# Performance work log

Measured on AMD Instinct MI355X. Metric: run time of the kernel, lower is better.

## Reference

```python
import jax, jax.numpy as jnp
import numpy as np

B, L, D, NLAYERS, KCONV = 8, 2048, 1024, 3, 4


def setup_inputs() -> dict:
    key = jax.random.key(0)
    ks = jax.random.split(key, 8)
    inp = {
        "x": jax.random.normal(ks[0], (B, L, D), jnp.float32),
        "conv_w": jax.random.normal(ks[1], (NLAYERS, D, KCONV), jnp.float32) * 0.02,
        "conv_b": jnp.zeros((NLAYERS, D), jnp.float32),
        "wr_w": jax.random.normal(ks[2], (NLAYERS, D, D), jnp.float32) * (1.0 / np.sqrt(D)),
        "wr_b": jnp.zeros((NLAYERS, D), jnp.float32),
        "wi_w": jax.random.normal(ks[3], (NLAYERS, D, D), jnp.float32) * (1.0 / np.sqrt(D)),
        "wi_b": jnp.zeros((NLAYERS, D), jnp.float32),
        "log_a": 3.0 + 0.1 * jax.random.normal(ks[4], (NLAYERS, D), jnp.float32),
        "wo_w": jax.random.normal(ks[5], (NLAYERS, D, D), jnp.float32) * (1.0 / np.sqrt(D)),
        "norm_w": jnp.ones((NLAYERS, D), jnp.float32),
        "norm_out_w": jnp.ones((D,), jnp.float32),
    }
    return inp


def _rmsnorm(x, w, eps=1e-6):
    return x * w * jax.lax.rsqrt(jnp.mean(x * x, axis=-1, keepdims=True) + eps)


def _parallel_scan(a, b):
    # h_t = a_t * h_{t-1} + b_t  via log-space prefix scan (h0 = 0)
    a32 = a.astype(jnp.float32)
    b32 = b.astype(jnp.float32)
    log_A = jnp.cumsum(jnp.log(jnp.maximum(a32, 1e-7)), axis=1)
    log_A = jnp.maximum(log_A, -80.0)  # a<=1 so log_A<=0 already
    A = jnp.exp(log_A)
    h = A * jnp.cumsum(b32 * jnp.exp(-log_A), axis=1)
    return h.astype(a.dtype)


def _rglru_layer(x, cw, cb, wrw, wrb, wiw, wib, la, wow, nw):
    # causal depthwise conv1d, kernel 4, left pad 3
    Lx = x.shape[1]
    xp = jnp.pad(x, ((0, 0), (KCONV - 1, 0), (0, 0)))
    x_conv = cb + sum(xp[:, k:k + Lx, :] * cw[:, k] for k in range(KCONV))
    r_t = jax.nn.sigmoid(x_conv @ wrw.T + wrb)
    i_t = jax.nn.sigmoid(x_conv @ wiw.T + wib)
    a_base = jax.nn.sigmoid(la.astype(jnp.float32)).astype(x.dtype)
    a_t = a_base ** (8.0 * r_t)
    b_t = jnp.sqrt(jnp.clip(1.0 - a_t * a_t, 1e-6, None)) * (i_t * x_conv)
    h = _parallel_scan(a_t, b_t)
    return _rmsnorm(h @ wow.T, nw)


def reference(x, conv_w, conv_b, wr_w, wr_b, wi_w, wi_b, log_a, wo_w, norm_w, norm_out_w):
    h = x
    for l in range(NLAYERS):
        h = _rglru_layer(h, conv_w[l], conv_b[l], wr_w[l], wr_b[l],
                         wi_w[l], wi_b[l], log_a[l], wo_w[l], norm_w[l])
    return _rmsnorm(h, norm_out_w)
```

## Files before the change

### kernel.cpp

```cpp
#include <hip/hip_runtime.h>
#include <type_traits>

#define BDIM 8
#define LDIM 2048
#define DDIM 1024
#define NL 3
#define K4 4
#define MDIM (BDIM * LDIM)
#define BK 64
#define NT (DDIM / BK)

typedef __bf16 bf16x8 __attribute__((ext_vector_type(8)));
typedef __bf16 bf16x4 __attribute__((ext_vector_type(4)));
typedef float f32x4 __attribute__((ext_vector_type(4)));
typedef const __attribute__((address_space(1))) void gvoid_t;
typedef __attribute__((address_space(3))) void svoid_t;

__device__ __forceinline__ void load16(const void* g, void* lds_uniform) {
    __builtin_amdgcn_global_load_lds((gvoid_t*)g, (svoid_t*)lds_uniform, 16, 0, 0);
}

#define SBAR()                                  \
    do {                                        \
        asm volatile("" ::: "memory");          \
        __builtin_amdgcn_s_barrier();           \
        asm volatile("" ::: "memory");          \
    } while (0)
#define WAITV(N) asm volatile("s_waitcnt vmcnt(" #N ")" ::: "memory")

__global__ void cvt_bf16(const float* __restrict__ s, __bf16* __restrict__ d, int n) {
    int i = blockIdx.x * 256 + threadIdx.x;
    if (i < n) d[i] = (__bf16)s[i];
}

__global__ __launch_bounds__(256) void cvt_interleave(const float* __restrict__ wr,
                                                      const float* __restrict__ wi,
                                                      __bf16* __restrict__ w2, int n) {
    int i = blockIdx.x * 256 + threadIdx.x;
    if (i >= n) return;
    int k = i & (DDIM - 1);
    int ld = i >> 10;
    int l = ld >> 10;
    int d = ld & (DDIM - 1);
    size_t base = ((size_t)l * 2 * DDIM + 2 * d) * DDIM + k;
    w2[base] = (__bf16)wr[i];
    w2[base + DDIM] = (__bf16)wi[i];
}

template <typename T>
__global__ __launch_bounds__(256) void conv_kernel(const T* __restrict__ X,
                                                   const float* __restrict__ cw,
                                                   const float* __restrict__ cb,
                                                   __bf16* __restrict__ XC) {
    int idx = blockIdx.x * 256 + threadIdx.x;
    int d = (idx & (DDIM / 4 - 1)) << 2;
    int t = (idx >> 8) & (LDIM - 1);
    int b = idx >> 19;
    float wv[4][4];
    *(float4*)wv[0] = ((const float4*)cw)[d + 0];
    *(float4*)wv[1] = ((const float4*)cw)[d + 1];
    *(float4*)wv[2] = ((const float4*)cw)[d + 2];
    *(float4*)wv[3] = ((const float4*)cw)[d + 3];
    float4 cbv = *(const float4*)(cb + d);
    float acc[4] = {cbv.x, cbv.y, cbv.z, cbv.w};
#pragma unroll
    for (int k = 0; k < K4; k++) {
        int tt = t + k - (K4 - 1);
        if (tt >= 0) {
            size_t off = ((size_t)(b * LDIM + tt) << 10) + d;
            float xv[4];
            if constexpr (std::is_same<T, float>::value) {
                float4 v = *(const float4*)(X + off);
                xv[0] = v.x; xv[1] = v.y; xv[2] = v.z; xv[3] = v.w;
            } else {
                bf16x4 v = *(const bf16x4*)(X + off);
                xv[0] = (float)v.x; xv[1] = (float)v.y; xv[2] = (float)v.z; xv[3] = (float)v.w;
            }
#pragma unroll
            for (int j = 0; j < 4; j++) acc[j] += xv[j] * wv[j][k];
        }
    }
    bf16x4 o;
    o.x = (__bf16)acc[0]; o.y = (__bf16)acc[1]; o.z = (__bf16)acc[2]; o.w = (__bf16)acc[3];
    *(bf16x4*)(XC + ((size_t)(b * LDIM + t) << 10) + d) = o;
}

__global__ __launch_bounds__(512, 2) void gate_gemm(
    const __bf16* __restrict__ A, const __bf16* __restrict__ W2,
    const float* __restrict__ wrb, const float* __restrict__ wib,
    const float* __restrict__ la,
    __bf16* __restrict__ LOGA, __bf16* __restrict__ BB) {
    __shared__ __attribute__((aligned(16))) __bf16 sm[4][16384];
    int tid = threadIdx.x;
    int wave = tid >> 6, lane = tid & 63;
    int wm = wave >> 2, wn = wave & 3;
    int fr = lane & 15, quad = lane >> 4;

    int nx = gridDim.x;
    int bid = blockIdx.y * nx + blockIdx.x;
    int cpx = (nx * gridDim.y) >> 3;
    int sw = (bid & 7) * cpx + (bid >> 3);
    int bm0 = (sw / nx) * 256;
    int bn0 = (sw % nx) * 256;

    const __bf16* Ag = A + (size_t)bm0 * DDIM;
    const __bf16* Bg = W2 + (size_t)bn0 * DDIM;

    f32x4 acc[8][4];
    f32x4 zero = {0.f, 0.f, 0.f, 0.f};
#pragma unroll
    for (int i = 0; i < 8; i++)
#pragma unroll
        for (int j = 0; j < 4; j++) acc[i][j] = zero;

    auto STAGE = [&](int buf, int ko) {
#pragma unroll
        for (int h = 0; h < 2; h++)
#pragma unroll
            for (int j = 0; j < 2; j++) {
                int ci = j * 512 + tid;
                int r = ci >> 3;
                int g = (ci & 7) ^ (r & 7);
                size_t go = (size_t)(h * 128 + r) * DDIM + ko + g * 8;
                int lb = h * 8192 + j * 4096 + wave * 512;
                load16(Ag + go, &sm[buf * 2][lb]);
                load16(Bg + go, &sm[buf * 2 + 1][lb]);
            }
    };

    STAGE(0, 0);
    int c = 0;
    for (int t = 0; t < NT; t++) {
        SBAR();
        if (t + 1 < NT) {
            STAGE(c ^ 1, (t + 1) * BK);
            WAITV(8);
        } else {
            WAITV(0);
        }
        SBAR();
        const __bf16* Ac = sm[c * 2];
        const __bf16* Bc = sm[c * 2 + 1];
#pragma unroll
        for (int ph = 0; ph < 4; ph++) {
            if (ph) SBAR();
            const int mh = ph & 1, kw = ph >> 1;
            bf16x8 af[4], bfm[4];
#pragma unroll
            for (int mi = 0; mi < 4; mi++) {
                int row = wm * 128 + (mh * 4 + mi) * 16 + fr;
                af[mi] = *(const bf16x8*)(Ac + row * 64 + ((kw * 4 + quad) ^ (row & 7)) * 8);
            }
#pragma unroll
            for (int ni = 0; ni < 4; ni++) {
                int row = wn * 64 + ni * 16 + fr;
                bfm[ni] = *(const bf16x8*)(Bc + row * 64 + ((kw * 4 + quad) ^ (row & 7)) * 8);
            }
            __builtin_amdgcn_s_setprio(1);
#pragma unroll
            for (int ni = 0; ni < 4; ni++)
#pragma unroll
                for (int mi = 0; mi < 4; mi++)
                    acc[mh * 4 + mi][ni] = __builtin_amdgcn_mfma_f32_16x16x32_bf16(
                        af[mi], bfm[ni], acc[mh * 4 + mi][ni], 0, 0, 0);
            __builtin_amdgcn_s_setprio(0);
        }
        c ^= 1;
    }

    float* Lt = (float*)&sm[0][0];
    int colg = (tid & 31) * 8;
    int d0 = (bn0 >> 1) + (colg >> 1);
    float rb[4], ibv[4], lnab[4];
    {
        float4 r4 = *(const float4*)(wrb + d0);
        float4 i4 = *(const float4*)(wib + d0);
        float4 l4 = *(const float4*)(la + d0);
        float lav[4] = {l4.x, l4.y, l4.z, l4.w};
        rb[0] = r4.x; rb[1] = r4.y; rb[2] = r4.z; rb[3] = r4.w;
        ibv[0] = i4.x; ibv[1] = i4.y; ibv[2] = i4.z; ibv[3] = i4.w;
#pragma unroll
        for (int j = 0; j < 4; j++) lnab[j] = __logf(1.f / (1.f + __expf(-lav[j])));
    }
#pragma unroll
    for (int mi = 0; mi < 8; mi++) {
        __syncthreads();
#pragma unroll
        for (int ni = 0; ni < 4; ni++) {
            int col = wn * 64 + ni * 16 + fr;
#pragma unroll
            for (int reg = 0; reg < 4; reg++)
                Lt[(wm * 16 + quad * 4 + reg) * 260 + col] = acc[mi][ni][reg];
        }
        __syncthreads();
#pragma unroll
        for (int hf = 0; hf < 2; hf++) {
            int r = (tid >> 5) + hf * 16;
            int m = bm0 + (r >> 4) * 128 + mi * 16 + (r & 15);
            float vv[8];
            *(f32x4*)&vv[0] = *(const f32x4*)&Lt[r * 260 + colg];
            *(f32x4*)&vv[4] = *(const f32x4*)&Lt[r * 260 + colg + 4];
            bf16x4 xcv = *(const bf16x4*)(A + (size_t)m * DDIM + d0);
            bf16x4 og, ob;
#pragma unroll
            for (int j = 0; j < 4; j++) {
                float rv = 1.f / (1.f + __expf(-(vv[2 * j] + rb[j])));
                float iv = 1.f / (1.f + __expf(-(vv[2 * j + 1] + ibv[j])));
                float lga = 8.f * rv * lnab[j];
                float a = __expf(lga);
                float bt = sqrtf(fmaxf(1.f - a * a, 1e-6f)) * (iv * (float)xcv[j]);
                og[j] = (__bf16)lga;
                ob[j] = (__bf16)bt;
            }
            *(bf16x4*)(LOGA + (size_t)m * DDIM + d0) = og;
            *(bf16x4*)(BB + (size_t)m * DDIM + d0) = ob;
        }
    }
}

__global__ __launch_bounds__(512, 2) void out_gemm(
    const __bf16* __restrict__ A, const __bf16* __restrict__ Wo, __bf16* __restrict__ HW) {
    __shared__ __attribute__((aligned(16))) __bf16 sm[4][16384];
    int tid = threadIdx.x;
    int wave = tid >> 6, lane = tid & 63;
    int wm = wave >> 2, wn = wave & 3;
    int fr = lane & 15, quad = lane >> 4;

    int nx = gridDim.x;
    int bid = blockIdx.y * nx + blockIdx.x;
    int cpx = (nx * gridDim.y) >> 3;
    int sw = (bid & 7) * cpx + (bid >> 3);
    int bm0 = (sw / nx) * 256;
    int bn0 = (sw % nx) * 256;

    const __bf16* Ag = A + (size_t)bm0 * DDIM;
    const __bf16* Bg = Wo + (size_t)bn0 * DDIM;

    f32x4 acc[8][4];
    f32x4 zero = {0.f, 0.f, 0.f, 0.f};
#pragma unroll
    for (int i = 0; i < 8; i++)
#pragma unroll
        for (int j = 0; j < 4; j++) acc[i][j] = zero;

    auto STAGE = [&](int buf, int ko) {
#pragma unroll
        for (int h = 0; h < 2; h++)
#pragma unroll
            for (int j = 0; j < 2; j++) {
                int ci = j * 512 + tid;
                int r = ci >> 3;
                int g = (ci & 7) ^ (r & 7);
                size_t go = (size_t)(h * 128 + r) * DDIM + ko + g * 8;
                int lb = h * 8192 + j * 4096 + wave * 512;
                load16(Ag + go, &sm[buf * 2][lb]);
                load16(Bg + go, &sm[buf * 2 + 1][lb]);
            }
    };

    STAGE(0, 0);
    int c = 0;
    for (int t = 0; t < NT; t++) {
        SBAR();
        if (t + 1 < NT) {
            STAGE(c ^ 1, (t + 1) * BK);
            WAITV(8);
        } else {
            WAITV(0);
        }
        SBAR();
        const __bf16* Ac = sm[c * 2];
        const __bf16* Bc = sm[c * 2 + 1];
#pragma unroll
        for (int ph = 0; ph < 4; ph++) {
            if (ph) SBAR();
            const int mh = ph & 1, kw = ph >> 1;
            bf16x8 af[4], bfm[4];
#pragma unroll
            for (int mi = 0; mi < 4; mi++) {
                int row = wm * 128 + (mh * 4 + mi) * 16 + fr;
                af[mi] = *(const bf16x8*)(Ac + row * 64 + ((kw * 4 + quad) ^ (row & 7)) * 8);
            }
#pragma unroll
            for (int ni = 0; ni < 4; ni++) {
                int row = wn * 64 + ni * 16 + fr;
                bfm[ni] = *(const bf16x8*)(Bc + row * 64 + ((kw * 4 + quad) ^ (row & 7)) * 8);
            }
            __builtin_amdgcn_s_setprio(1);
#pragma unroll
            for (int ni = 0; ni < 4; ni++)
#pragma unroll
                for (int mi = 0; mi < 4; mi++)
                    acc[mh * 4 + mi][ni] = __builtin_amdgcn_mfma_f32_16x16x32_bf16(
                        af[mi], bfm[ni], acc[mh * 4 + mi][ni], 0, 0, 0);
            __builtin_amdgcn_s_setprio(0);
        }
        c ^= 1;
    }

    float* Lt = (float*)&sm[0][0];
    int colg = (tid & 31) * 8;
    int n0 = bn0 + colg;
#pragma unroll
    for (int mi = 0; mi < 8; mi++) {
        __syncthreads();
#pragma unroll
        for (int ni = 0; ni < 4; ni++) {
            int col = wn * 64 + ni * 16 + fr;
#pragma unroll
            for (int reg = 0; reg < 4; reg++)
                Lt[(wm * 16 + quad * 4 + reg) * 260 + col] = acc[mi][ni][reg];
        }
        __syncthreads();
#pragma unroll
        for (int hf = 0; hf < 2; hf++) {
            int r = (tid >> 5) + hf * 16;
            int m = bm0 + (r >> 4) * 128 + mi * 16 + (r & 15);
            float vv[8];
            *(f32x4*)&vv[0] = *(const f32x4*)&Lt[r * 260 + colg];
            *(f32x4*)&vv[4] = *(const f32x4*)&Lt[r * 260 + colg + 4];
            bf16x8 o;
#pragma unroll
            for (int j = 0; j < 8; j++) o[j] = (__bf16)vv[j];
            *(bf16x8*)(HW + (size_t)m * DDIM + n0) = o;
        }
    }
}

#define SC_T (LDIM / 8)
__global__ __launch_bounds__(256) void scan_kernel(const __bf16* __restrict__ LOGA,
                                                   const __bf16* __restrict__ BB,
                                                   __bf16* __restrict__ H) {
    int b = blockIdx.y;
    int dl = threadIdx.x & 31;
    int d = blockIdx.x * 32 + dl;
    int c = threadIdx.x >> 5;
    size_t base = ((size_t)b * LDIM + (size_t)c * SC_T) * DDIM + d;
    const __bf16* pga = LOGA + base;
    const __bf16* pbb = BB + base;
    __bf16* pH = H + base;

    float S = 0.f;
#pragma unroll 8
    for (int t = 0; t < SC_T; t++) S += (float)pga[(size_t)t * DDIM];
    __shared__ float sS[8][32];
    sS[c][dl] = S;
    __syncthreads();
    float L0 = 0.f;
    for (int cc = 0; cc < c; cc++) L0 += sS[cc][dl];

    float Lr = L0, lcp = fmaxf(L0, -80.f), hB = 0.f;
#pragma unroll 4
    for (int t = 0; t < SC_T; t++) {
        float lga = (float)pga[(size_t)t * DDIM];
        Lr += lga;
        float lc = fmaxf(Lr, -80.f);
        hB = __expf(lc - lcp) * hB + (float)pbb[(size_t)t * DDIM];
        lcp = lc;
    }
    float Ac = __expf(fmaxf(Lr, -80.f) - fmaxf(L0, -80.f));
    __shared__ float sA[8][32], sB[8][32];
    sA[c][dl] = Ac;
    sB[c][dl] = hB;
    __syncthreads();
    float hin = 0.f;
    for (int cc = 0; cc < c; cc++) hin = sA[cc][dl] * hin + sB[cc][dl];

    Lr = L0;
    lcp = fmaxf(L0, -80.f);
    float h = hin;
#pragma unroll 4
    for (int t = 0; t < SC_T; t++) {
        float lga = (float)pga[(size_t)t * DDIM];
        Lr += lga;
        float lc = fmaxf(Lr, -80.f);
        h = __expf(lc - lcp) * h + (float)pbb[(size_t)t * DDIM];
        lcp = lc;
        pH[(size_t)t * DDIM] = (__bf16)h;
    }
}

template <typename TI, typename TO>
__global__ __launch_bounds__(256) void rmsnorm_kernel(const TI* __restrict__ X,
                                                      const float* __restrict__ w,
                                                      TO* __restrict__ Y) {
    int row = blockIdx.x;
    int tid = threadIdx.x;
    size_t off = (size_t)row * DDIM + tid * 4;
    float v[4];
    if constexpr (std::is_same<TI, float>::value) {
        float4 t = *(const float4*)(X + off);
        v[0] = t.x; v[1] = t.y; v[2] = t.z; v[3] = t.w;
    } else {
        bf16x4 t = *(const bf16x4*)(X + off);
        v[0] = (float)t.x; v[1] = (float)t.y; v[2] = (float)t.z; v[3] = (float)t.w;
    }
    float s = v[0] * v[0] + v[1] * v[1] + v[2] * v[2] + v[3] * v[3];
#pragma unroll
    for (int o = 32; o > 0; o >>= 1) s += __shfl_down(s, o);
    __shared__ float sw[4];
    if ((tid & 63) == 0) sw[tid >> 6] = s;
    __syncthreads();
    float tot = sw[0] + sw[1] + sw[2] + sw[3];
    float scale = rsqrtf(tot * (1.f / (float)DDIM) + 1e-6f);
    float4 wv = ((const float4*)w)[tid];
    float o0 = v[0] * wv.x * scale, o1 = v[1] * wv.y * scale;
    float o2 = v[2] * wv.z * scale, o3 = v[3] * wv.w * scale;
    if constexpr (std::is_same<TO, float>::value) {
        float4 o = {o0, o1, o2, o3};
        *(float4*)(Y + off) = o;
    } else {
        bf16x4 o;
        o.x = (__bf16)o0; o.y = (__bf16)o1; o.z = (__bf16)o2; o.w = (__bf16)o3;
        *(bf16x4*)(Y + off) = o;
    }
}

extern "C" void kernel_launch(void* const* d_in, const int* in_sizes, int n_in,
                              void* d_out, int out_size, void* d_ws, size_t ws_size,
                              hipStream_t stream) {
    const float* x = (const float*)d_in[0];
    const float* conv_w = (const float*)d_in[1];
    const float* conv_b = (const float*)d_in[2];
    const float* wr_w = (const float*)d_in[3];
    const float* wr_b = (const float*)d_in[4];
    const float* wi_w = (const float*)d_in[5];
    const float* wi_b = (const float*)d_in[6];
    const float* log_a = (const float*)d_in[7];
    const float* wo_w = (const float*)d_in[8];
    const float* norm_w = (const float*)d_in[9];
    const float* norm_out_w = (const float*)d_in[10];

    const size_t W2SZ = (size_t)NL * 2 * DDIM * DDIM;
    const size_t WOSZ = (size_t)NL * DDIM * DDIM;
    const size_t MD = (size_t)MDIM * DDIM;
    __bf16* w2 = (__bf16*)d_ws;
    __bf16* wo16 = w2 + W2SZ;
    __bf16* XC = wo16 + WOSZ;
    __bf16* LGA = XC + MD;
    __bf16* BBf = LGA + MD;
    __bf16* Hb = BBf + MD;
    __bf16* HWb = Hb + MD;
    __bf16* PNb = HWb + MD;

    int nw = (int)WOSZ;
    cvt_interleave<<<(nw + 255) / 256, 256, 0, stream>>>(wr_w, wi_w, w2, nw);
    cvt_bf16<<<(nw + 255) / 256, 256, 0, stream>>>(wo_w, wo16, nw);

    for (int l = 0; l < NL; l++) {
        if (l == 0)
            conv_kernel<float><<<(MDIM * (DDIM / 4)) / 256, 256, 0, stream>>>(
                x, conv_w, conv_b, XC);
        else
            conv_kernel<__bf16><<<(MDIM * (DDIM / 4)) / 256, 256, 0, stream>>>(
                PNb, conv_w + (size_t)l * DDIM * K4, conv_b + (size_t)l * DDIM, XC);
        gate_gemm<<<dim3(2 * DDIM / 256, MDIM / 256), 512, 0, stream>>>(
            XC, w2 + (size_t)l * 2 * DDIM * DDIM,
            wr_b + (size_t)l * DDIM, wi_b + (size_t)l * DDIM, log_a + (size_t)l * DDIM,
            LGA, BBf);
        scan_kernel<<<dim3(DDIM / 32, BDIM), 256, 0, stream>>>(LGA, BBf, Hb);
        out_gemm<<<dim3(DDIM / 256, MDIM / 256), 512, 0, stream>>>(
            Hb, wo16 + (size_t)l * DDIM * DDIM, HWb);
        rmsnorm_kernel<__bf16, __bf16><<<MDIM, 256, 0, stream>>>(
            HWb, norm_w + (size_t)l * DDIM, PNb);
    }
    rmsnorm_kernel<__bf16, float><<<MDIM, 256, 0, stream>>>(PNb, norm_out_w, (float*)d_out);
}
```

Baseline: 1.021 ms.

## Switch GEMM mainloops to 4-stage BK=32 pipeline with single barrier per step

Result: no change. 1.004 ms (-1.7%).

```diff
diff --git a/kernel.cpp b/kernel.cpp
--- a/kernel.cpp
+++ b/kernel.cpp
@@ -7,8 +7,8 @@
 #define NL 3
 #define K4 4
 #define MDIM (BDIM * LDIM)
-#define BK 64
-#define NT (DDIM / BK)
+#define BK32 32
+#define NT32 (DDIM / BK32)
 
 typedef __bf16 bf16x8 __attribute__((ext_vector_type(8)));
 typedef __bf16 bf16x4 __attribute__((ext_vector_type(4)));
@@ -90,7 +90,7 @@
     const float* __restrict__ wrb, const float* __restrict__ wib,
     const float* __restrict__ la,
     __bf16* __restrict__ LOGA, __bf16* __restrict__ BB) {
-    __shared__ __attribute__((aligned(16))) __bf16 sm[4][16384];
+    __shared__ __attribute__((aligned(16))) __bf16 sm[4][2][8192];
     int tid = threadIdx.x;
     int wave = tid >> 6, lane = tid & 63;
     int wm = wave >> 2, wn = wave & 3;
@@ -115,60 +115,58 @@
 
     auto STAGE = [&](int buf, int ko) {
 #pragma unroll
-        for (int h = 0; h < 2; h++)
-#pragma unroll
-            for (int j = 0; j < 2; j++) {
-                int ci = j * 512 + tid;
-                int r = ci >> 3;
-                int g = (ci & 7) ^ (r & 7);
-                size_t go = (size_t)(h * 128 + r) * DDIM + ko + g * 8;
-                int lb = h * 8192 + j * 4096 + wave * 512;
-                load16(Ag + go, &sm[buf * 2][lb]);
-                load16(Bg + go, &sm[buf * 2 + 1][lb]);
-            }
+        for (int j = 0; j < 2; j++) {
+            int ci = j * 512 + tid;
+            int r = ci >> 2;
+            int g = (ci & 3) ^ ((r >> 1) & 3);
+            size_t go = (size_t)r * DDIM + ko + g * 8;
+            int lb = j * 4096 + wave * 512;
+            load16(Ag + go, &sm[buf][0][lb]);
+            load16(Bg + go, &sm[buf][1][lb]);
+        }
     };
 
     STAGE(0, 0);
-    int c = 0;
-    for (int t = 0; t < NT; t++) {
-        SBAR();
-        if (t + 1 < NT) {
-            STAGE(c ^ 1, (t + 1) * BK);
-            WAITV(8);
-        } else {
-            WAITV(0);
-        }
-        SBAR();
-        const __bf16* Ac = sm[c * 2];
-        const __bf16* Bc = sm[c * 2 + 1];
-#pragma unroll
-        for (int ph = 0; ph < 4; ph++) {
-            if (ph) SBAR();
-            const int mh = ph & 1, kw = ph >> 1;
-            bf16x8 af[4], bfm[4];
-#pragma unroll
-            for (int mi = 0; mi < 4; mi++) {
-                int row = wm * 128 + (mh * 4 + mi) * 16 + fr;
-                af[mi] = *(const bf16x8*)(Ac + row * 64 + ((kw * 4 + quad) ^ (row & 7)) * 8);
-            }
+    STAGE(1, BK32);
+    STAGE(2, 2 * BK32);
+    for (int t4 = 0; t4 < NT32; t4 += 4) {
+#pragma unroll
+        for (int tt = 0; tt < 4; tt++) {
+            int t = t4 + tt;
+            if (t + 2 < NT32) { WAITV(8); }
+            else if (t + 1 < NT32) { WAITV(4); }
+            else { WAITV(0); }
+            SBAR();
+            if (t + 3 < NT32) STAGE((tt + 3) & 3, (t + 3) * BK32);
+            const __bf16* Ac = &sm[tt][0][0];
+            const __bf16* Bc = &sm[tt][1][0];
+            bf16x8 bfm[4];
 #pragma unroll
             for (int ni = 0; ni < 4; ni++) {
                 int row = wn * 64 + ni * 16 + fr;
-                bfm[ni] = *(const bf16x8*)(Bc + row * 64 + ((kw * 4 + quad) ^ (row & 7)) * 8);
-            }
-            __builtin_amdgcn_s_setprio(1);
-#pragma unroll
-            for (int ni = 0; ni < 4; ni++)
-#pragma unroll
-                for (int mi = 0; mi < 4; mi++)
-                    acc[mh * 4 + mi][ni] = __builtin_amdgcn_mfma_f32_16x16x32_bf16(
-                        af[mi], bfm[ni], acc[mh * 4 + mi][ni], 0, 0, 0);
-            __builtin_amdgcn_s_setprio(0);
-        }
-        c ^= 1;
-    }
-
-    float* Lt = (float*)&sm[0][0];
+                bfm[ni] = *(const bf16x8*)(Bc + row * 32 + ((quad ^ ((row >> 1) & 3)) << 3));
+            }
+#pragma unroll
+            for (int mh = 0; mh < 2; mh++) {
+                bf16x8 af[4];
+#pragma unroll
+                for (int mi = 0; mi < 4; mi++) {
+                    int row = wm * 128 + (mh * 4 + mi) * 16 + fr;
+                    af[mi] = *(const bf16x8*)(Ac + row * 32 + ((quad ^ ((row >> 1) & 3)) << 3));
+                }
+                __builtin_amdgcn_s_setprio(1);
+#pragma unroll
+                for (int ni = 0; ni < 4; ni++)
+#pragma unroll
+                    for (int mi = 0; mi < 4; mi++)
+                        acc[mh * 4 + mi][ni] = __builtin_amdgcn_mfma_f32_16x16x32_bf16(
+                            af[mi], bfm[ni], acc[mh * 4 + mi][ni], 0, 0, 0);
+                __builtin_amdgcn_s_setprio(0);
+            }
+        }
+    }
+
+    float* Lt = (float*)&sm[0][0][0];
     int colg = (tid & 31) * 8;
     int d0 = (bn0 >> 1) + (colg >> 1);
     float rb[4], ibv[4], lnab[4];
@@ -220,7 +218,7 @@
 
 __global__ __launch_bounds__(512, 2) void out_gemm(
     const __bf16* __restrict__ A, const __bf16* __restrict__ Wo, __bf16* __restrict__ HW) {
-    __shared__ __attribute__((aligned(16))) __bf16 sm[4][16384];
+    __shared__ __attribute__((aligned(16))) __bf16 sm[4][2][8192];
     int tid = threadIdx.x;
     int wave = tid >> 6, lane = tid & 63;
     int wm = wave >> 2, wn = wave & 3;
@@ -245,60 +243,58 @@
 
     auto STAGE = [&](int buf, int ko) {
 #pragma unroll
-        for (int h = 0; h < 2; h++)
-#pragma unroll
-            for (int j = 0; j < 2; j++) {
-                int ci = j * 512 + tid;
-                int r = ci >> 3;
-                int g = (ci & 7) ^ (r & 7);
-                size_t go = (size_t)(h * 128 + r) * DDIM + ko + g * 8;
-                int lb = h * 8192 + j * 4096 + wave * 512;
-                load16(Ag + go, &sm[buf * 2][lb]);
-                load16(Bg + go, &sm[buf * 2 + 1][lb]);
-            }
+        for (int j = 0; j < 2; j++) {
+            int ci = j * 512 + tid;
+            int r = ci >> 2;
+            int g = (ci & 3) ^ ((r >> 1) & 3);
+            size_t go = (size_t)r * DDIM + ko + g * 8;
+            int lb = j * 4096 + wave * 512;
+            load16(Ag + go, &sm[buf][0][lb]);
+            load16(Bg + go, &sm[buf][1][lb]);
+        }
     };
 
     STAGE(0, 0);
-    int c = 0;
-    for (int t = 0; t < NT; t++) {
-        SBAR();
-        if (t + 1 < NT) {
-            STAGE(c ^ 1, (t + 1) * BK);
-            WAITV(8);
-        } else {
-            WAITV(0);
-        }
-        SBAR();
-        const __bf16* Ac = sm[c * 2];
-        const __bf16* Bc = sm[c * 2 + 1];
-#pragma unroll
-        for (int ph = 0; ph < 4; ph++) {
-            if (ph) SBAR();
-            const int mh = ph & 1, kw = ph >> 1;
-            bf16x8 af[4], bfm[4];
-#pragma unroll
-            for (int mi = 0; mi < 4; mi++) {
-                int row = wm * 128 + (mh * 4 + mi) * 16 + fr;
-                af[mi] = *(const bf16x8*)(Ac + row * 64 + ((kw * 4 + quad) ^ (row & 7)) * 8);
-            }
+    STAGE(1, BK32);
+    STAGE(2, 2 * BK32);
+    for (int t4 = 0; t4 < NT32; t4 += 4) {
+#pragma unroll
+        for (int tt = 0; tt < 4; tt++) {
+            int t = t4 + tt;
+            if (t + 2 < NT32) { WAITV(8); }
+            else if (t + 1 < NT32) { WAITV(4); }
+            else { WAITV(0); }
+            SBAR();
+            if (t + 3 < NT32) STAGE((tt + 3) & 3, (t + 3) * BK32);
+            const __bf16* Ac = &sm[tt][0][0];
+            const __bf16* Bc = &sm[tt][1][0];
+            bf16x8 bfm[4];
 #pragma unroll
             for (int ni = 0; ni < 4; ni++) {
                 int row = wn * 64 + ni * 16 + fr;
-                bfm[ni] = *(const bf16x8*)(Bc + row * 64 + ((kw * 4 + quad) ^ (row & 7)) * 8);
-            }
-            __builtin_amdgcn_s_setprio(1);
-#pragma unroll
-            for (int ni = 0; ni < 4; ni++)
-#pragma unroll
-                for (int mi = 0; mi < 4; mi++)
-                    acc[mh * 4 + mi][ni] = __builtin_amdgcn_mfma_f32_16x16x32_bf16(
-                        af[mi], bfm[ni], acc[mh * 4 + mi][ni], 0, 0, 0);
-            __builtin_amdgcn_s_setprio(0);
-        }
-        c ^= 1;
-    }
-
-    float* Lt = (float*)&sm[0][0];
+                bfm[ni] = *(const bf16x8*)(Bc + row * 32 + ((quad ^ ((row >> 1) & 3)) << 3));
+            }
+#pragma unroll
+            for (int mh = 0; mh < 2; mh++) {
+                bf16x8 af[4];
+#pragma unroll
+                for (int mi = 0; mi < 4; mi++) {
+                    int row = wm * 128 + (mh * 4 + mi) * 16 + fr;
+                    af[mi] = *(const bf16x8*)(Ac + row * 32 + ((quad ^ ((row >> 1) & 3)) << 3));
+                }
+                __builtin_amdgcn_s_setprio(1);
+#pragma unroll
+                for (int ni = 0; ni < 4; ni++)
+#pragma unroll
+                    for (int mi = 0; mi < 4; mi++)
+                        acc[mh * 4 + mi][ni] = __builtin_amdgcn_mfma_f32_16x16x32_bf16(
+                            af[mi], bfm[ni], acc[mh * 4 + mi][ni], 0, 0, 0);
+                __builtin_amdgcn_s_setprio(0);
+            }
+        }
+    }
+
+    float* Lt = (float*)&sm[0][0][0];
     int colg = (tid & 31) * 8;
     int n0 = bn0 + colg;
 #pragma unroll
```
